# Kernel optimization log

Measured on AMD Instinct MI355X. Metric: run time of the kernel, lower is better.

Reference implementation:

```python
import jax, jax.numpy as jnp
import numpy as np

EDGE_R = 7                      # box-filter radius -> 15x15 all-ones kernel
EBT_BALANCE = (1.0, 0.8, 0.5)   # Edge / Boundary-band / Texture balance
LAYER_WEIGHT = 1.0              # single (non-list) prediction path


def setup_inputs() -> dict:
    key = jax.random.key(0)
    k1, k2 = jax.random.split(key)
    b, c, h, w = 16, 1, 1024, 1024
    # Pred are probabilities (module applies BCELoss directly); keep away from {0,1}
    Pred = jax.random.uniform(k1, (b, c, h, w), jnp.float32, 0.01, 0.99)
    label = jax.random.randint(k2, (b, c, h, w), 0, 2).astype(jnp.int32)
    return {"Pred": Pred, "label": label}


def _ebt_loss(Pred, label_f):
    b, c, h, w = label_f.shape
    num_total = float(b * c * h * w)
    mask = jnp.clip(label_f, 0.0, 1.0)
    k = 2 * EDGE_R + 1
    filt = jnp.ones((1, 1, k, k), mask.dtype)
    # 15x15 all-ones box filter with 'same' padding (edge dilation of the mask)
    edge = jax.lax.conv_general_dilated(
        mask, filt, window_strides=(1, 1),
        padding=[(EDGE_R, EDGE_R), (EDGE_R, EDGE_R)],
        dimension_numbers=("NCHW", "OIHW", "NCHW"))
    edge = jnp.where(edge > 0, 1.0, 0.0)  # binarize (conv output is >= 0)
    B = edge - label_f           # boundary band around foreground
    T = 1.0 - edge               # texture (far-from-edge background)
    num_E = mask.sum()
    num_B = B.sum()
    num_T = T.sum()
    weight = ((1.0 - num_E / num_total) * EBT_BALANCE[0] * mask
              + (1.0 - num_B / num_total) * EBT_BALANCE[1] * B
              + (1.0 - num_T / num_total) * EBT_BALANCE[2] * T)
    # BCELoss(reduction='none'): -(t*log(p) + (1-t)*log(1-p))
    bce = -(label_f * jnp.log(Pred) + (1.0 - label_f) * jnp.log1p(-Pred))
    return (weight * bce).mean()


def reference(Pred, label):
    label_f = label.astype(jnp.float32)
    return LAYER_WEIGHT * _ebt_loss(Pred, label_f)
```

## Files before the change

kernel.cpp:

```cpp
#include <hip/hip_runtime.h>
#include <math.h>

#define IMG_H 1024
#define IMG_W 1024
#define NB    16
#define NROWS (NB * IMG_H)
#define WPR   (IMG_W / 32)
#define NTOTAL 16777216.0
#define NBUCKET 1024
#define LN2 0.6931471805599453

struct Acc {
    double s2A, s2E, s2M;
    unsigned int cMask, cEdge;
};

__global__ void k_dilate_h(const int* __restrict__ label,
                           unsigned int* __restrict__ maskbits,
                           unsigned int* __restrict__ rowor,
                           Acc* __restrict__ acc) {
    __shared__ unsigned int lm[256];
    const int t = threadIdx.x;
    const long rowBase = (long)blockIdx.x * 8;
    const long pixBase = rowBase * IMG_W;

    if (blockIdx.x < NBUCKET && t < 8)
        ((unsigned int*)&acc[blockIdx.x])[t] = 0u;

    const int4* L = (const int4*)(label + pixBase);
    #pragma unroll
    for (int k = 0; k < 8; ++k) {
        const int fi = k * 256 + t;
        const int4 v = L[fi];
        unsigned int wbits = ((unsigned int)(v.x & 1)
                           | ((unsigned int)(v.y & 1) << 1)
                           | ((unsigned int)(v.z & 1) << 2)
                           | ((unsigned int)(v.w & 1) << 3)) << ((t & 7) * 4);
        wbits |= __shfl_xor(wbits, 1);
        wbits |= __shfl_xor(wbits, 2);
        wbits |= __shfl_xor(wbits, 4);
        if ((t & 7) == 0) lm[fi >> 3] = wbits;
    }
    __syncthreads();

    const int wd = t & 31;
    unsigned int prev = wd        ? lm[t - 1] : 0u;
    unsigned int cur  =             lm[t];
    unsigned int next = (wd < 31) ? lm[t + 1] : 0u;
    unsigned long long Wn = (((unsigned long long)prev) >> 16)
                          | (((unsigned long long)cur)  << 16)
                          | (((unsigned long long)next) << 48);
    unsigned long long a = Wn;
    #pragma unroll
    for (int d = 1; d <= 7; ++d) a |= (Wn >> d) | (Wn << d);

    long o = rowBase * WPR + t;
    maskbits[o] = cur;
    rowor[o]    = (unsigned int)(a >> 16);
}

__global__ void k_bce(const float* __restrict__ pred,
                      const unsigned int* __restrict__ maskbits,
                      const unsigned int* __restrict__ rowor,
                      Acc* __restrict__ acc) {
    __shared__ unsigned int eM[256], eE[256];
    __shared__ float redf[12];
    __shared__ unsigned int redc[8];

    const int t  = threadIdx.x;
    const int R0 = blockIdx.x * 8;
    const int b  = R0 >> 10;
    const int i0 = R0 & 1023;

    const int g = t >> 5, w = t & 31;
    {
        const int i = i0 + g;
        int lo = i - 7; if (lo < 0) lo = 0;
        int hi = i + 7; if (hi > 1023) hi = 1023;
        const unsigned int* base = rowor + ((long)b << 10) * WPR + w;
        unsigned int e = 0u;
        for (int ri = lo; ri <= hi; ++ri) e |= base[(long)ri * WPR];
        eE[t] = e;
        eM[t] = maskbits[(long)(R0 + g) * WPR + w];
    }
    unsigned int cM = __popc(eM[t]), cE = __popc(eE[t]);
    __syncthreads();

    float s2A = 0.f, s2E = 0.f, s2M = 0.f;
    const float4* p4 = (const float4*)(pred + (long)R0 * IMG_W);
    #pragma unroll
    for (int k = 0; k < 8; ++k) {
        const int f = t + k * 256;
        const float4 pv = p4[f];
        const unsigned int sh = (f & 7) << 2;
        const unsigned int mN = (eM[f >> 3] >> sh) & 0xFu;
        const unsigned int eN = (eE[f >> 3] >> sh) & 0xFu;
        const float pj[4] = {pv.x, pv.y, pv.z, pv.w};
        #pragma unroll
        for (int j = 0; j < 4; ++j) {
            const unsigned int m = (mN >> j) & 1u;
            const unsigned int e = (eN >> j) & 1u;
            const float x = m ? pj[j] : 1.0f - pj[j];
            const float l = __log2f(x);
            s2A += l;
            s2E += e ? l : 0.f;
            s2M += m ? l : 0.f;
        }
    }

    #pragma unroll
    for (int off = 32; off; off >>= 1) {
        s2A += __shfl_down(s2A, off);
        s2E += __shfl_down(s2E, off);
        s2M += __shfl_down(s2M, off);
        cM  += __shfl_down(cM, off);
        cE  += __shfl_down(cE, off);
    }
    const int wave = t >> 6, lane = t & 63;
    if (lane == 0) {
        redf[wave * 3 + 0] = s2A;
        redf[wave * 3 + 1] = s2E;
        redf[wave * 3 + 2] = s2M;
        redc[wave * 2 + 0] = cM;
        redc[wave * 2 + 1] = cE;
    }
    __syncthreads();
    if (t == 0) {
        float tA = 0.f, tEg = 0.f, tMg = 0.f;
        unsigned int tM = 0, tEd = 0;
        #pragma unroll
        for (int wv = 0; wv < 4; ++wv) {
            tA  += redf[wv * 3 + 0];
            tEg += redf[wv * 3 + 1];
            tMg += redf[wv * 3 + 2];
            tM  += redc[wv * 2 + 0];
            tEd += redc[wv * 2 + 1];
        }
        Acc* a = &acc[blockIdx.x & (NBUCKET - 1)];
        atomicAdd(&a->s2A, (double)tA);
        atomicAdd(&a->s2E, (double)tEg);
        atomicAdd(&a->s2M, (double)tMg);
        atomicAdd(&a->cMask, tM);
        atomicAdd(&a->cEdge, tEd);
    }
}

__global__ void k_final(const Acc* __restrict__ acc, float* __restrict__ out) {
    __shared__ double redd[12];
    __shared__ double redn[8];
    const int t = threadIdx.x;
    double sA = 0.0, sEg = 0.0, sMg = 0.0, nM = 0.0, nEd = 0.0;
    for (int idx = t; idx < NBUCKET; idx += 256) {
        sA  += acc[idx].s2A;  sEg += acc[idx].s2E;  sMg += acc[idx].s2M;
        nM  += (double)acc[idx].cMask;  nEd += (double)acc[idx].cEdge;
    }
    #pragma unroll
    for (int off = 32; off; off >>= 1) {
        sA  += __shfl_down(sA, off);
        sEg += __shfl_down(sEg, off);
        sMg += __shfl_down(sMg, off);
        nM  += __shfl_down(nM, off);
        nEd += __shfl_down(nEd, off);
    }
    const int wave = t >> 6, lane = t & 63;
    if (lane == 0) {
        redd[wave * 3 + 0] = sA;
        redd[wave * 3 + 1] = sEg;
        redd[wave * 3 + 2] = sMg;
        redn[wave * 2 + 0] = nM;
        redn[wave * 2 + 1] = nEd;
    }
    __syncthreads();
    if (t == 0) {
        double tA = 0, tEg = 0, tMg = 0, tM = 0, tEd = 0;
        #pragma unroll
        for (int wv = 0; wv < 4; ++wv) {
            tA  += redd[wv * 3 + 0];
            tEg += redd[wv * 3 + 1];
            tMg += redd[wv * 3 + 2];
            tM  += redn[wv * 2 + 0];
            tEd += redn[wv * 2 + 1];
        }
        double sE_bce = -LN2 * tMg;
        double sEdge  = -LN2 * tEg;
        double sAll   = -LN2 * tA;
        double sB_bce = sEdge - sE_bce;
        double sT_bce = sAll - sEdge;
        double nBnd = tEd - tM;
        double nT   = NTOTAL - tEd;
        double wE = (1.0 - tM   / NTOTAL) * 1.0;
        double wB = (1.0 - nBnd / NTOTAL) * 0.8;
        double wT = (1.0 - nT   / NTOTAL) * 0.5;
        out[0] = (float)((wE * sE_bce + wB * sB_bce + wT * sT_bce) / NTOTAL);
    }
}

extern "C" void kernel_launch(void* const* d_in, const int* in_sizes, int n_in,
                              void* d_out, int out_size, void* d_ws, size_t ws_size,
                              hipStream_t stream) {
    const float* pred  = (const float*)d_in[0];
    const int*   label = (const int*)d_in[1];
    float* out = (float*)d_out;

    char* ws = (char*)d_ws;
    Acc* acc = (Acc*)ws;
    unsigned int* maskbits = (unsigned int*)(ws + (size_t)NBUCKET * sizeof(Acc));
    unsigned int* rowor    = (unsigned int*)(ws + (size_t)NBUCKET * sizeof(Acc)
                                               + (size_t)NROWS * WPR * 4);

    k_dilate_h<<<NROWS / 8, 256, 0, stream>>>(label, maskbits, rowor, acc);
    k_bce<<<NROWS / 8, 256, 0, stream>>>(pred, maskbits, rowor, acc);
    k_final<<<1, 256, 0, stream>>>(acc, out);
}
```

Before: 148.8 us.

## Swap dilation order and fold final reduction into last BCE block

The label kernel now only packs mask bits. The BCE kernel does the vertical OR over packed rows first and then the horizontal 15-wide dilation in shared memory, which removes the separate row-OR buffer write and read. The single-block final kernel is dropped: a completion counter lets the last BCE block do the final reduction, which saves one launch. The risk is an extra barrier and a little more work per block, plus correctness that depends on the threadfence and atomic ordering.

```diff
diff --git a/kernel.cpp b/kernel.cpp
--- a/kernel.cpp
+++ b/kernel.cpp
@@ -15,19 +15,20 @@
     unsigned int cMask, cEdge;
 };
 
-__global__ void k_dilate_h(const int* __restrict__ label,
-                           unsigned int* __restrict__ maskbits,
-                           unsigned int* __restrict__ rowor,
-                           Acc* __restrict__ acc) {
+__global__ void k_pack(const int* __restrict__ label,
+                       unsigned int* __restrict__ maskbits,
+                       Acc* __restrict__ acc,
+                       unsigned int* __restrict__ done) {
     __shared__ unsigned int lm[256];
     const int t = threadIdx.x;
     const long rowBase = (long)blockIdx.x * 8;
-    const long pixBase = rowBase * IMG_W;
 
     if (blockIdx.x < NBUCKET && t < 8)
         ((unsigned int*)&acc[blockIdx.x])[t] = 0u;
-
-    const int4* L = (const int4*)(label + pixBase);
+    if (blockIdx.x == 0 && t == 8)
+        *done = 0u;
+
+    const int4* L = (const int4*)(label + rowBase * IMG_W);
     #pragma unroll
     for (int k = 0; k < 8; ++k) {
         const int fi = k * 256 + t;
@@ -42,48 +43,57 @@
         if ((t & 7) == 0) lm[fi >> 3] = wbits;
     }
     __syncthreads();
-
-    const int wd = t & 31;
-    unsigned int prev = wd        ? lm[t - 1] : 0u;
-    unsigned int cur  =             lm[t];
-    unsigned int next = (wd < 31) ? lm[t + 1] : 0u;
-    unsigned long long Wn = (((unsigned long long)prev) >> 16)
-                          | (((unsigned long long)cur)  << 16)
-                          | (((unsigned long long)next) << 48);
-    unsigned long long a = Wn;
-    #pragma unroll
-    for (int d = 1; d <= 7; ++d) a |= (Wn >> d) | (Wn << d);
-
-    long o = rowBase * WPR + t;
-    maskbits[o] = cur;
-    rowor[o]    = (unsigned int)(a >> 16);
+    maskbits[rowBase * WPR + t] = lm[t];
 }
 
 __global__ void k_bce(const float* __restrict__ pred,
                       const unsigned int* __restrict__ maskbits,
-                      const unsigned int* __restrict__ rowor,
-                      Acc* __restrict__ acc) {
-    __shared__ unsigned int eM[256], eE[256];
+                      Acc* __restrict__ acc,
+                      unsigned int* __restrict__ done,
+                      float* __restrict__ out) {
+    __shared__ unsigned int vE[256];
+    __shared__ unsigned int eE[256];
+    __shared__ unsigned int eM[256];
     __shared__ float redf[12];
     __shared__ unsigned int redc[8];
+    __shared__ double redd[12];
+    __shared__ double redn[8];
+    __shared__ int lastFlag;
 
     const int t  = threadIdx.x;
     const int R0 = blockIdx.x * 8;
     const int b  = R0 >> 10;
     const int i0 = R0 & 1023;
-
     const int g = t >> 5, w = t & 31;
+
     {
         const int i = i0 + g;
         int lo = i - 7; if (lo < 0) lo = 0;
         int hi = i + 7; if (hi > 1023) hi = 1023;
-        const unsigned int* base = rowor + ((long)b << 10) * WPR + w;
+        const unsigned int* base = maskbits + ((long)b << 10) * WPR + w;
         unsigned int e = 0u;
         for (int ri = lo; ri <= hi; ++ri) e |= base[(long)ri * WPR];
-        eE[t] = e;
-        eM[t] = maskbits[(long)(R0 + g) * WPR + w];
-    }
-    unsigned int cM = __popc(eM[t]), cE = __popc(eE[t]);
+        vE[t] = e;
+        eM[t] = base[(long)i * WPR];
+    }
+    __syncthreads();
+
+    unsigned int cE;
+    {
+        unsigned int prev = w        ? vE[t - 1] : 0u;
+        unsigned int cur  =            vE[t];
+        unsigned int next = (w < 31) ? vE[t + 1] : 0u;
+        unsigned long long Wn = (((unsigned long long)prev) >> 16)
+                              | (((unsigned long long)cur)  << 16)
+                              | (((unsigned long long)next) << 48);
+        unsigned long long a = Wn;
+        #pragma unroll
+        for (int d = 1; d <= 7; ++d) a |= (Wn >> d) | (Wn << d);
+        unsigned int ew = (unsigned int)(a >> 16);
+        eE[t] = ew;
+        cE = __popc(ew);
+    }
+    unsigned int cM = __popc(eM[t]);
     __syncthreads();
 
     float s2A = 0.f, s2E = 0.f, s2M = 0.f;
@@ -142,56 +152,60 @@
         atomicAdd(&a->s2M, (double)tMg);
         atomicAdd(&a->cMask, tM);
         atomicAdd(&a->cEdge, tEd);
-    }
-}
-
-__global__ void k_final(const Acc* __restrict__ acc, float* __restrict__ out) {
-    __shared__ double redd[12];
-    __shared__ double redn[8];
-    const int t = threadIdx.x;
-    double sA = 0.0, sEg = 0.0, sMg = 0.0, nM = 0.0, nEd = 0.0;
-    for (int idx = t; idx < NBUCKET; idx += 256) {
-        sA  += acc[idx].s2A;  sEg += acc[idx].s2E;  sMg += acc[idx].s2M;
-        nM  += (double)acc[idx].cMask;  nEd += (double)acc[idx].cEdge;
-    }
-    #pragma unroll
-    for (int off = 32; off; off >>= 1) {
-        sA  += __shfl_down(sA, off);
-        sEg += __shfl_down(sEg, off);
-        sMg += __shfl_down(sMg, off);
-        nM  += __shfl_down(nM, off);
-        nEd += __shfl_down(nEd, off);
-    }
-    const int wave = t >> 6, lane = t & 63;
-    if (lane == 0) {
-        redd[wave * 3 + 0] = sA;
-        redd[wave * 3 + 1] = sEg;
-        redd[wave * 3 + 2] = sMg;
-        redn[wave * 2 + 0] = nM;
-        redn[wave * 2 + 1] = nEd;
-    }
-    __syncthreads();
-    if (t == 0) {
-        double tA = 0, tEg = 0, tMg = 0, tM = 0, tEd = 0;
-        #pragma unroll
-        for (int wv = 0; wv < 4; ++wv) {
-            tA  += redd[wv * 3 + 0];
-            tEg += redd[wv * 3 + 1];
-            tMg += redd[wv * 3 + 2];
-            tM  += redn[wv * 2 + 0];
-            tEd += redn[wv * 2 + 1];
-        }
-        double sE_bce = -LN2 * tMg;
-        double sEdge  = -LN2 * tEg;
-        double sAll   = -LN2 * tA;
-        double sB_bce = sEdge - sE_bce;
-        double sT_bce = sAll - sEdge;
-        double nBnd = tEd - tM;
-        double nT   = NTOTAL - tEd;
-        double wE = (1.0 - tM   / NTOTAL) * 1.0;
-        double wB = (1.0 - nBnd / NTOTAL) * 0.8;
-        double wT = (1.0 - nT   / NTOTAL) * 0.5;
-        out[0] = (float)((wE * sE_bce + wB * sB_bce + wT * sT_bce) / NTOTAL);
+        __threadfence();
+        unsigned int old = atomicAdd(done, 1u);
+        lastFlag = (old == (unsigned int)(gridDim.x - 1)) ? 1 : 0;
+    }
+    __syncthreads();
+
+    if (lastFlag) {
+        __threadfence();
+        double sA = 0.0, sEg = 0.0, sMg = 0.0, nM = 0.0, nEd = 0.0;
+        for (int idx = t; idx < NBUCKET; idx += 256) {
+            sA  += __hip_atomic_load(&acc[idx].s2A, __ATOMIC_RELAXED, __HIP_MEMORY_SCOPE_AGENT);
+            sEg += __hip_atomic_load(&acc[idx].s2E, __ATOMIC_RELAXED, __HIP_MEMORY_SCOPE_AGENT);
+            sMg += __hip_atomic_load(&acc[idx].s2M, __ATOMIC_RELAXED, __HIP_MEMORY_SCOPE_AGENT);
+            nM  += (double)__hip_atomic_load(&acc[idx].cMask, __ATOMIC_RELAXED, __HIP_MEMORY_SCOPE_AGENT);
+            nEd += (double)__hip_atomic_load(&acc[idx].cEdge, __ATOMIC_RELAXED, __HIP_MEMORY_SCOPE_AGENT);
+        }
+        #pragma unroll
+        for (int off = 32; off; off >>= 1) {
+            sA  += __shfl_down(sA, off);
+            sEg += __shfl_down(sEg, off);
+            sMg += __shfl_down(sMg, off);
+            nM  += __shfl_down(nM, off);
+            nEd += __shfl_down(nEd, off);
+        }
+        if (lane == 0) {
+            redd[wave * 3 + 0] = sA;
+            redd[wave * 3 + 1] = sEg;
+            redd[wave * 3 + 2] = sMg;
+            redn[wave * 2 + 0] = nM;
+            redn[wave * 2 + 1] = nEd;
+        }
+        __syncthreads();
+        if (t == 0) {
+            double tA = 0, tEg = 0, tMg = 0, tM = 0, tEd = 0;
+            #pragma unroll
+            for (int wv = 0; wv < 4; ++wv) {
+                tA  += redd[wv * 3 + 0];
+                tEg += redd[wv * 3 + 1];
+                tMg += redd[wv * 3 + 2];
+                tM  += redn[wv * 2 + 0];
+                tEd += redn[wv * 2 + 1];
+            }
+            double sE_bce = -LN2 * tMg;
+            double sEdge  = -LN2 * tEg;
+            double sAll   = -LN2 * tA;
+            double sB_bce = sEdge - sE_bce;
+            double sT_bce = sAll - sEdge;
+            double nBnd = tEd - tM;
+            double nT   = NTOTAL - tEd;
+            double wE = (1.0 - tM   / NTOTAL) * 1.0;
+            double wB = (1.0 - nBnd / NTOTAL) * 0.8;
+            double wT = (1.0 - nT   / NTOTAL) * 0.5;
+            out[0] = (float)((wE * sE_bce + wB * sB_bce + wT * sT_bce) / NTOTAL);
+        }
     }
 }
 
@@ -205,10 +219,9 @@
     char* ws = (char*)d_ws;
     Acc* acc = (Acc*)ws;
     unsigned int* maskbits = (unsigned int*)(ws + (size_t)NBUCKET * sizeof(Acc));
-    unsigned int* rowor    = (unsigned int*)(ws + (size_t)NBUCKET * sizeof(Acc)
+    unsigned int* done     = (unsigned int*)(ws + (size_t)NBUCKET * sizeof(Acc)
                                                + (size_t)NROWS * WPR * 4);
 
-    k_dilate_h<<<NROWS / 8, 256, 0, stream>>>(label, maskbits, rowor, acc);
-    k_bce<<<NROWS / 8, 256, 0, stream>>>(pred, maskbits, rowor, acc);
-    k_final<<<1, 256, 0, stream>>>(acc, out);
+    k_pack<<<NROWS / 8, 256, 0, stream>>>(label, maskbits, acc, done);
+    k_bce<<<NROWS / 8, 256, 0, stream>>>(pred, maskbits, acc, done, out);
 }
```

Measured after the change: 223.9 us. 1.5x slower.
